# Kernel optimization log

Hardware: AMD Instinct MI355X
Metric: run time of the kernel (lower is better)

The kernel has to match this reference:

```python
import jax, jax.numpy as jnp
import numpy as np

B, N_IN, D = 2, 262144, 32
N_OUT, K, NK = 65536, 4, 9
MIN_DIST = 0.01


def setup_inputs() -> dict:
    key = jax.random.key(0)
    k1, k2, k3, k4 = jax.random.split(key, 4)
    x_level_in = jax.random.normal(k1, (B, N_IN, D), dtype=jnp.float32)
    coords_in = jax.random.uniform(k2, (2, B, N_IN), dtype=jnp.float32)
    coords_out = jax.random.uniform(k3, (2, B, N_OUT, K), dtype=jnp.float32)
    neighbor_idx = jax.random.randint(k4, (B, N_OUT, K, NK), 0, N_IN)
    sigma = jnp.ones((D,), dtype=jnp.float32) * (MIN_DIST * 200.0)
    return {
        "x_level_in": x_level_in,
        "coords_in": coords_in,
        "coords_out": coords_out,
        "sigma": sigma,
        "neighbor_idx": neighbor_idx,
    }


def reference(x_level_in, coords_in, coords_out, sigma, neighbor_idx):
    # x_level_in: [B, N_in, D]; coords_in: [2, B, N_in]
    # coords_out: [2, B, N_out, K]; neighbor_idx: [B, N_out, K, NK]; sigma: [D]
    b = jnp.arange(x_level_in.shape[0])[:, None, None, None]  # batch index broadcaster
    # gather neighbor coordinates across the input grid: [2, B, N_out, K, NK]
    nb_coords = coords_in[:, b, neighbor_idx]
    # squared euclidean distance in (lon, lat): [B, N_out, K, NK]
    d2 = jnp.sum((coords_out[..., None] - nb_coords) ** 2, axis=0)
    # per-channel Gaussian/RBF weights: [B, N_out, K, NK, D]
    w = jnp.exp(-d2[..., None] / (2.0 * sigma ** 2))
    # gather neighbor features: [B, N_out, K, NK, D]
    feats = x_level_in[b, neighbor_idx]
    # normalized weighted aggregate over the NK neighbors: [B, N_out, K, D]
    num = jnp.sum(w * feats, axis=3)
    den = jnp.sum(w, axis=3) + 1e-9
    x = num / den
    # flatten (N_out, K) -> sequence dim, as in forward's final view
    return x.reshape(x.shape[0], -1, x.shape[-1])
```

## Files before the change

kernel.cpp:

```cpp
#include <hip/hip_runtime.h>
#include <hip/hip_fp16.h>

constexpr int B        = 2;
constexpr int N_IN     = 262144;
constexpr int D        = 32;
constexpr int N_OUT    = 65536;
constexpr int K        = 4;
constexpr int NK       = 9;
constexpr int P        = B * N_OUT * K;
constexpr int PPB      = N_OUT * K;
constexpr size_t XTOT  = (size_t)B * N_IN * D;

typedef _Float16 half4v __attribute__((ext_vector_type(4)));
typedef _Float16 half8v __attribute__((ext_vector_type(8)));

__global__ __launch_bounds__(256) void cvt_fp16_kernel(
    const float* __restrict__ x, _Float16* __restrict__ xh)
{
    const size_t i = (size_t)(blockIdx.x * 256 + threadIdx.x) * 8;
    const float4 a = *reinterpret_cast<const float4*>(x + i);
    const float4 b = *reinterpret_cast<const float4*>(x + i + 4);
    half8v h;
    h[0] = (_Float16)a.x; h[1] = (_Float16)a.y;
    h[2] = (_Float16)a.z; h[3] = (_Float16)a.w;
    h[4] = (_Float16)b.x; h[5] = (_Float16)b.y;
    h[6] = (_Float16)b.z; h[7] = (_Float16)b.w;
    *reinterpret_cast<half8v*>(xh + i) = h;
}

__global__ __launch_bounds__(256) void pack_coords_kernel(
    const float* __restrict__ cin, float2* __restrict__ cp)
{
    const int i = blockIdx.x * 256 + threadIdx.x;
    cp[i] = make_float2(cin[i], cin[B * N_IN + i]);
}

__global__ __launch_bounds__(256) void projection_kernel_h(
    const _Float16* __restrict__ xh,
    const float2*   __restrict__ cpack,
    const float*    __restrict__ coords_out,
    const float*    __restrict__ sigma,
    const int*      __restrict__ nidx,
    float*          __restrict__ out)
{
    const int bid   = blockIdx.x;
    const int xcd   = bid & 7;
    const int j     = bid >> 3;
    const int batch = xcd >> 2;
    const int bbi   = j * 4 + (xcd & 3);
    const int point = batch * PPB + bbi * 32 + (threadIdx.x >> 3);
    const int q     = threadIdx.x & 7;

    const int cbase = batch * N_IN;

    const float cox = coords_out[point];
    const float coy = coords_out[P + point];

    const float4 sg = *reinterpret_cast<const float4*>(sigma + q * 4);
    const float s0 = 1.0f / (2.0f * sg.x * sg.x);
    const float s1 = 1.0f / (2.0f * sg.y * sg.y);
    const float s2 = 1.0f / (2.0f * sg.z * sg.z);
    const float s3 = 1.0f / (2.0f * sg.w * sg.w);
    const bool uni = (sg.x == sg.y) && (sg.y == sg.z) && (sg.z == sg.w);

    int idxs[NK];
    const int* __restrict__ ip = nidx + (size_t)point * NK;
    #pragma unroll
    for (int t = 0; t < NK; ++t) idxs[t] = ip[t];

    float2 c[NK];
    #pragma unroll
    for (int t = 0; t < NK; ++t) c[t] = cpack[cbase + idxs[t]];

    half4v f[NK];
    #pragma unroll
    for (int t = 0; t < NK; ++t)
        f[t] = *reinterpret_cast<const half4v*>(
            xh + (size_t)(cbase + idxs[t]) * D + q * 4);

    float4 num = make_float4(0.f, 0.f, 0.f, 0.f);
    float4 den = make_float4(0.f, 0.f, 0.f, 0.f);

    if (uni) {
        #pragma unroll
        for (int t = 0; t < NK; ++t) {
            const float dx = cox - c[t].x;
            const float dy = coy - c[t].y;
            const float d2 = dx * dx + dy * dy;
            const float w  = __expf(-d2 * s0);
            num.x += w * (float)f[t][0];
            num.y += w * (float)f[t][1];
            num.z += w * (float)f[t][2];
            num.w += w * (float)f[t][3];
            den.x += w;
        }
        den.y = den.x; den.z = den.x; den.w = den.x;
    } else {
        #pragma unroll
        for (int t = 0; t < NK; ++t) {
            const float dx = cox - c[t].x;
            const float dy = coy - c[t].y;
            const float d2 = dx * dx + dy * dy;
            const float w0 = __expf(-d2 * s0);
            const float w1 = __expf(-d2 * s1);
            const float w2 = __expf(-d2 * s2);
            const float w3 = __expf(-d2 * s3);
            num.x += w0 * (float)f[t][0];  den.x += w0;
            num.y += w1 * (float)f[t][1];  den.y += w1;
            num.z += w2 * (float)f[t][2];  den.z += w2;
            num.w += w3 * (float)f[t][3];  den.w += w3;
        }
    }

    float4 o;
    o.x = num.x / (den.x + 1e-9f);
    o.y = num.y / (den.y + 1e-9f);
    o.z = num.z / (den.z + 1e-9f);
    o.w = num.w / (den.w + 1e-9f);

    *reinterpret_cast<float4*>(out + (size_t)point * D + q * 4) = o;
}

__global__ __launch_bounds__(256) void projection_kernel_f32(
    const float* __restrict__ x,
    const float* __restrict__ coords_in,
    const float* __restrict__ coords_out,
    const float* __restrict__ sigma,
    const int*   __restrict__ nidx,
    float*       __restrict__ out)
{
    const int tid   = blockIdx.x * 256 + threadIdx.x;
    const int point = tid >> 3;
    const int q     = tid & 7;
    const int b     = point / PPB;
    const int cbase = b * N_IN;

    const float cox = coords_out[point];
    const float coy = coords_out[P + point];

    const float4 sg = *reinterpret_cast<const float4*>(sigma + q * 4);
    const float s0 = 1.0f / (2.0f * sg.x * sg.x);
    const float s1 = 1.0f / (2.0f * sg.y * sg.y);
    const float s2 = 1.0f / (2.0f * sg.z * sg.z);
    const float s3 = 1.0f / (2.0f * sg.w * sg.w);

    float4 num = make_float4(0.f, 0.f, 0.f, 0.f);
    float4 den = make_float4(0.f, 0.f, 0.f, 0.f);
    const int* __restrict__ ip = nidx + (size_t)point * NK;

    #pragma unroll
    for (int nk = 0; nk < NK; ++nk) {
        const int idx = ip[nk];
        const float cx = coords_in[cbase + idx];
        const float cy = coords_in[B * N_IN + cbase + idx];
        const float dx = cox - cx;
        const float dy = coy - cy;
        const float d2 = dx * dx + dy * dy;
        const float4 f = *reinterpret_cast<const float4*>(
            x + (size_t)(cbase + idx) * D + q * 4);
        const float w0 = __expf(-d2 * s0);
        const float w1 = __expf(-d2 * s1);
        const float w2 = __expf(-d2 * s2);
        const float w3 = __expf(-d2 * s3);
        num.x += w0 * f.x;  den.x += w0;
        num.y += w1 * f.y;  den.y += w1;
        num.z += w2 * f.z;  den.z += w2;
        num.w += w3 * f.w;  den.w += w3;
    }

    float4 o;
    o.x = num.x / (den.x + 1e-9f);
    o.y = num.y / (den.y + 1e-9f);
    o.z = num.z / (den.z + 1e-9f);
    o.w = num.w / (den.w + 1e-9f);
    *reinterpret_cast<float4*>(out + (size_t)point * D + q * 4) = o;
}

extern "C" void kernel_launch(void* const* d_in, const int* in_sizes, int n_in,
                              void* d_out, int out_size, void* d_ws, size_t ws_size,
                              hipStream_t stream) {
    const float* x      = (const float*)d_in[0];
    const float* cin    = (const float*)d_in[1];
    const float* cout_  = (const float*)d_in[2];
    const float* sigma  = (const float*)d_in[3];
    const int*   nidx   = (const int*)  d_in[4];
    float*       outp   = (float*)d_out;

    const int block = 256;
    const int grid_main = (P * 8) / block;

    const size_t xh_bytes = XTOT * sizeof(_Float16);
    const size_t cp_bytes = (size_t)B * N_IN * sizeof(float2);

    if (ws_size >= xh_bytes + cp_bytes) {
        _Float16* xh = (_Float16*)d_ws;
        float2*   cp = (float2*)((char*)d_ws + xh_bytes);
        cvt_fp16_kernel<<<(int)(XTOT / 8 / block), block, 0, stream>>>(x, xh);
        pack_coords_kernel<<<(B * N_IN) / block, block, 0, stream>>>(cin, cp);
        projection_kernel_h<<<grid_main, block, 0, stream>>>(
            xh, cp, cout_, sigma, nidx, outp);
    } else {
        projection_kernel_f32<<<grid_main, block, 0, stream>>>(
            x, cin, cout_, sigma, nidx, outp);
    }
}
```

Measured before the change: 238.5 us.

## Use 4 threads per point with 16-byte half8 gathers and fp16 packed coords

Each output point is now handled by 4 threads instead of 8. Each thread gathers 8 fp16 channels with a 16-byte load and writes two float4 outputs. The packed input coordinates are stored as fp16 pairs rather than float2, which halves the coordinate gather size and the workspace it needs. Index and coords_out reads and output writes now use nontemporal hints. The aim is to cut redundant index and coordinate loads and the number of memory transactions, at some risk to coordinate precision and with more registers per thread.

```diff
diff --git a/kernel.cpp b/kernel.cpp
--- a/kernel.cpp
+++ b/kernel.cpp
@@ -11,8 +11,9 @@
 constexpr int PPB      = N_OUT * K;
 constexpr size_t XTOT  = (size_t)B * N_IN * D;
 
-typedef _Float16 half4v __attribute__((ext_vector_type(4)));
+typedef _Float16 half2v __attribute__((ext_vector_type(2)));
 typedef _Float16 half8v __attribute__((ext_vector_type(8)));
+typedef float    f4v    __attribute__((ext_vector_type(4)));
 
 __global__ __launch_bounds__(256) void cvt_fp16_kernel(
     const float* __restrict__ x, _Float16* __restrict__ xh)
@@ -29,15 +30,18 @@
 }
 
 __global__ __launch_bounds__(256) void pack_coords_kernel(
-    const float* __restrict__ cin, float2* __restrict__ cp)
+    const float* __restrict__ cin, half2v* __restrict__ cp)
 {
     const int i = blockIdx.x * 256 + threadIdx.x;
-    cp[i] = make_float2(cin[i], cin[B * N_IN + i]);
+    half2v h;
+    h[0] = (_Float16)cin[i];
+    h[1] = (_Float16)cin[B * N_IN + i];
+    cp[i] = h;
 }
 
 __global__ __launch_bounds__(256) void projection_kernel_h(
     const _Float16* __restrict__ xh,
-    const float2*   __restrict__ cpack,
+    const half2v*   __restrict__ cpack,
     const float*    __restrict__ coords_out,
     const float*    __restrict__ sigma,
     const int*      __restrict__ nidx,
@@ -48,77 +52,83 @@
     const int j     = bid >> 3;
     const int batch = xcd >> 2;
     const int bbi   = j * 4 + (xcd & 3);
-    const int point = batch * PPB + bbi * 32 + (threadIdx.x >> 3);
-    const int q     = threadIdx.x & 7;
+    const int point = batch * PPB + bbi * 64 + (threadIdx.x >> 2);
+    const int h     = threadIdx.x & 3;
 
     const int cbase = batch * N_IN;
 
-    const float cox = coords_out[point];
-    const float coy = coords_out[P + point];
-
-    const float4 sg = *reinterpret_cast<const float4*>(sigma + q * 4);
-    const float s0 = 1.0f / (2.0f * sg.x * sg.x);
-    const float s1 = 1.0f / (2.0f * sg.y * sg.y);
-    const float s2 = 1.0f / (2.0f * sg.z * sg.z);
-    const float s3 = 1.0f / (2.0f * sg.w * sg.w);
-    const bool uni = (sg.x == sg.y) && (sg.y == sg.z) && (sg.z == sg.w);
+    const float cox = __builtin_nontemporal_load(coords_out + point);
+    const float coy = __builtin_nontemporal_load(coords_out + P + point);
+
+    const float4 sg0 = *reinterpret_cast<const float4*>(sigma + h * 8);
+    const float4 sg1 = *reinterpret_cast<const float4*>(sigma + h * 8 + 4);
+    float s[8];
+    s[0] = 1.0f / (2.0f * sg0.x * sg0.x); s[1] = 1.0f / (2.0f * sg0.y * sg0.y);
+    s[2] = 1.0f / (2.0f * sg0.z * sg0.z); s[3] = 1.0f / (2.0f * sg0.w * sg0.w);
+    s[4] = 1.0f / (2.0f * sg1.x * sg1.x); s[5] = 1.0f / (2.0f * sg1.y * sg1.y);
+    s[6] = 1.0f / (2.0f * sg1.z * sg1.z); s[7] = 1.0f / (2.0f * sg1.w * sg1.w);
+    bool uni = true;
+    #pragma unroll
+    for (int k = 1; k < 8; ++k) uni = uni && (s[k] == s[0]);
 
     int idxs[NK];
     const int* __restrict__ ip = nidx + (size_t)point * NK;
     #pragma unroll
-    for (int t = 0; t < NK; ++t) idxs[t] = ip[t];
-
-    float2 c[NK];
+    for (int t = 0; t < NK; ++t) idxs[t] = __builtin_nontemporal_load(ip + t);
+
+    half2v c[NK];
     #pragma unroll
     for (int t = 0; t < NK; ++t) c[t] = cpack[cbase + idxs[t]];
 
-    half4v f[NK];
+    half8v f[NK];
     #pragma unroll
     for (int t = 0; t < NK; ++t)
-        f[t] = *reinterpret_cast<const half4v*>(
-            xh + (size_t)(cbase + idxs[t]) * D + q * 4);
-
-    float4 num = make_float4(0.f, 0.f, 0.f, 0.f);
-    float4 den = make_float4(0.f, 0.f, 0.f, 0.f);
+        f[t] = *reinterpret_cast<const half8v*>(
+            xh + (size_t)(cbase + idxs[t]) * D + h * 8);
+
+    float num[8];
+    #pragma unroll
+    for (int k = 0; k < 8; ++k) num[k] = 0.f;
+
+    float den[8];
+    #pragma unroll
+    for (int k = 0; k < 8; ++k) den[k] = 0.f;
 
     if (uni) {
         #pragma unroll
         for (int t = 0; t < NK; ++t) {
-            const float dx = cox - c[t].x;
-            const float dy = coy - c[t].y;
-            const float d2 = dx * dx + dy * dy;
-            const float w  = __expf(-d2 * s0);
-            num.x += w * (float)f[t][0];
-            num.y += w * (float)f[t][1];
-            num.z += w * (float)f[t][2];
-            num.w += w * (float)f[t][3];
-            den.x += w;
+            const float dx = cox - (float)c[t][0];
+            const float dy = coy - (float)c[t][1];
+            const float w  = __expf(-(dx * dx + dy * dy) * s[0]);
+            den[0] += w;
+            #pragma unroll
+            for (int k = 0; k < 8; ++k) num[k] += w * (float)f[t][k];
         }
-        den.y = den.x; den.z = den.x; den.w = den.x;
+        #pragma unroll
+        for (int k = 1; k < 8; ++k) den[k] = den[0];
     } else {
         #pragma unroll
         for (int t = 0; t < NK; ++t) {
-            const float dx = cox - c[t].x;
-            const float dy = coy - c[t].y;
+            const float dx = cox - (float)c[t][0];
+            const float dy = coy - (float)c[t][1];
             const float d2 = dx * dx + dy * dy;
-            const float w0 = __expf(-d2 * s0);
-            const float w1 = __expf(-d2 * s1);
-            const float w2 = __expf(-d2 * s2);
-            const float w3 = __expf(-d2 * s3);
-            num.x += w0 * (float)f[t][0];  den.x += w0;
-            num.y += w1 * (float)f[t][1];  den.y += w1;
-            num.z += w2 * (float)f[t][2];  den.z += w2;
-            num.w += w3 * (float)f[t][3];  den.w += w3;
+            #pragma unroll
+            for (int k = 0; k < 8; ++k) {
+                const float w = __expf(-d2 * s[k]);
+                num[k] += w * (float)f[t][k];
+                den[k] += w;
+            }
         }
     }
 
-    float4 o;
-    o.x = num.x / (den.x + 1e-9f);
-    o.y = num.y / (den.y + 1e-9f);
-    o.z = num.z / (den.z + 1e-9f);
-    o.w = num.w / (den.w + 1e-9f);
-
-    *reinterpret_cast<float4*>(out + (size_t)point * D + q * 4) = o;
+    float* op = out + (size_t)point * D + h * 8;
+    f4v o0, o1;
+    o0.x = num[0] / (den[0] + 1e-9f); o0.y = num[1] / (den[1] + 1e-9f);
+    o0.z = num[2] / (den[2] + 1e-9f); o0.w = num[3] / (den[3] + 1e-9f);
+    o1.x = num[4] / (den[4] + 1e-9f); o1.y = num[5] / (den[5] + 1e-9f);
+    o1.z = num[6] / (den[6] + 1e-9f); o1.w = num[7] / (den[7] + 1e-9f);
+    __builtin_nontemporal_store(o0, reinterpret_cast<f4v*>(op));
+    __builtin_nontemporal_store(o1, reinterpret_cast<f4v*>(op + 4));
 }
 
 __global__ __launch_bounds__(256) void projection_kernel_f32(
@@ -187,19 +197,20 @@
     float*       outp   = (float*)d_out;
 
     const int block = 256;
-    const int grid_main = (P * 8) / block;
 
     const size_t xh_bytes = XTOT * sizeof(_Float16);
-    const size_t cp_bytes = (size_t)B * N_IN * sizeof(float2);
+    const size_t cp_bytes = (size_t)B * N_IN * sizeof(half2v);
 
     if (ws_size >= xh_bytes + cp_bytes) {
         _Float16* xh = (_Float16*)d_ws;
-        float2*   cp = (float2*)((char*)d_ws + xh_bytes);
+        half2v*   cp = (half2v*)((char*)d_ws + xh_bytes);
         cvt_fp16_kernel<<<(int)(XTOT / 8 / block), block, 0, stream>>>(x, xh);
         pack_coords_kernel<<<(B * N_IN) / block, block, 0, stream>>>(cin, cp);
+        const int grid_main = (P * 4) / block;
         projection_kernel_h<<<grid_main, block, 0, stream>>>(
             xh, cp, cout_, sigma, nidx, outp);
     } else {
+        const int grid_main = (P * 8) / block;
         projection_kernel_f32<<<grid_main, block, 0, stream>>>(
             x, cin, cout_, sigma, nidx, outp);
     }
```

New measurement: 218.4 us. 1.09x faster.
